# Kernel optimization log

Measured on AMD Instinct MI355X. Metric: run time of the kernel, lower is better.

## Reference

```python
import jax, jax.numpy as jnp
import numpy as np

N_NODES = 50000
N_EDGES = 800000
NFEAT, NHID, NCLASS = 512, 128, 40


def _glorot(key, fan_in, fan_out):
    # mimics the usual GCN uniform init: U(-1/sqrt(fan_out), 1/sqrt(fan_out))
    stdv = 1.0 / np.sqrt(fan_out)
    return jax.random.uniform(key, (fan_in, fan_out), jnp.float32, -stdv, stdv)


def setup_inputs() -> dict:
    key = jax.random.key(0)
    ks = jax.random.split(key, 8)
    x = jax.random.normal(ks[0], (N_NODES, NFEAT), jnp.float32)
    edge_src = jax.random.randint(ks[1], (N_EDGES,), 0, N_NODES)
    edge_dst = jax.random.randint(ks[2], (N_EDGES,), 0, N_NODES)
    edge_weight = jax.random.uniform(ks[3], (N_EDGES,), jnp.float32)
    W1 = _glorot(ks[4], NFEAT, NHID)
    b1 = jnp.zeros((NHID,), jnp.float32)
    W2 = _glorot(ks[5], NHID, NCLASS)
    b2 = jnp.zeros((NCLASS,), jnp.float32)
    return {"x": x, "edge_src": edge_src, "edge_dst": edge_dst,
            "edge_weight": edge_weight, "W1": W1, "b1": b1, "W2": W2, "b2": b2}


def _gcn_layer(x, W, b, edge_src, edge_dst, edge_weight):
    # support = x @ W ; out = spmm(adj, support) + b
    support = x @ W                                   # [N, F_out]
    msgs = support[edge_src] * edge_weight[:, None]   # [E, F_out]
    agg = jax.ops.segment_sum(msgs, edge_dst, num_segments=N_NODES)
    return agg + b


def reference(x, edge_src, edge_dst, edge_weight, W1, b1, W2, b2):
    h = _gcn_layer(x, W1, b1, edge_src, edge_dst, edge_weight)
    h = jax.nn.relu(h)
    # F.dropout(training=False) -> identity in eval mode
    out = _gcn_layer(h, W2, b2, edge_src, edge_dst, edge_weight)
    return out
```

## Files before the change

### kernel.cpp

```cpp
#include <hip/hip_runtime.h>


#define F0 512
#define F1 128
#define F2 40
#define F2P 48

typedef short bf16x8 __attribute__((ext_vector_type(8)));
typedef float f32x4 __attribute__((ext_vector_type(4)));

static __device__ __forceinline__ unsigned short f2b(float f){
    union { float f; unsigned int u; } x; x.f = f;
    unsigned int u = x.u;
    unsigned int r = (u + 0x7fffu + ((u >> 16) & 1u)) >> 16;
    return (unsigned short)r;
}
static __device__ __forceinline__ unsigned short f2b_fast(float f){
    return (unsigned short)((__float_as_uint(f) + 0x8000u) >> 16);
}
static __device__ __forceinline__ unsigned int pack2(float a, float b){
    unsigned int ua = __float_as_uint(a) + 0x8000u;
    unsigned int ub = __float_as_uint(b) + 0x8000u;
    return __builtin_amdgcn_perm(ub, ua, 0x07060302u);
}
static __device__ __forceinline__ bf16x8 pack8(float4 v0, float4 v1){
    union { bf16x8 v; unsigned int d[4]; } r;
    r.d[0] = pack2(v0.x, v0.y);
    r.d[1] = pack2(v0.z, v0.w);
    r.d[2] = pack2(v1.x, v1.y);
    r.d[3] = pack2(v1.z, v1.w);
    return r.v;
}
static __device__ __forceinline__ float b2f(unsigned short h){
    union { unsigned int u; float f; } x; x.u = ((unsigned int)h) << 16; return x.f;
}
static __device__ __forceinline__ unsigned short f2h(float f){
    union { _Float16 h; unsigned short u; } x; x.h = (_Float16)f; return x.u;
}
static __device__ __forceinline__ float h2f(unsigned short u){
    union { unsigned short u; _Float16 h; } x; x.u = u; return (float)x.h;
}

__global__ void prep_w(const float* __restrict__ W1, const float* __restrict__ W2,
                       unsigned short* __restrict__ W1t, unsigned short* __restrict__ W2t,
                       int* __restrict__ cnt8, int n8, int* __restrict__ gflag){
    int idx = blockIdx.x*256 + threadIdx.x;
    if (idx < n8) cnt8[idx] = 0;
    if (idx < 64) gflag[idx] = 0;
    if (idx < F0*F1){
        int k = idx >> 7, n = idx & 127;
        W1t[(size_t)n*F0 + k] = f2b(W1[idx]);
    } else if (idx < F0*F1 + F2P*F1){
        int j = idx - F0*F1;
        int n = j >> 7, k = j & 127;
        float v = (n < F2) ? W2[(size_t)k*F2 + n] : 0.f;
        W2t[j] = f2b(v);
    }
}

__global__ __launch_bounds__(256, 3) void gemm1h(const float* __restrict__ X,
                                                 const unsigned short* __restrict__ W1t,
                                                 unsigned short* __restrict__ S1, int M,
                                                 const int* __restrict__ dst,
                                                 int* __restrict__ cnt8,
                                                 unsigned short* __restrict__ slot,
                                                 int E, int epb){
    __shared__ unsigned short sB[128*136];
    int tid = threadIdx.x;
    int wave = tid >> 6, lane = tid & 63;
    int quad = lane >> 4, l16 = lane & 15;
    int row0 = blockIdx.x * 64;
    int myrow = row0 + wave*16 + l16;
    int arow = min(myrow, M-1);
    const float* xrow = X + (size_t)arow * F0;

    bf16x8 a[16];
    #pragma unroll
    for (int t=0; t<16; t++){
        float4 v0 = *(const float4*)(xrow + t*32 + quad*8);
        float4 v1 = *(const float4*)(xrow + t*32 + quad*8 + 4);
        a[t] = pack8(v0, v1);
    }
    __builtin_amdgcn_sched_barrier(0);

    f32x4 acc[8];
    #pragma unroll
    for (int c=0;c<8;c++) acc[c] = (f32x4){0.f,0.f,0.f,0.f};

    #pragma unroll
    for (int p = 0; p < 4; p++){
        __syncthreads();
        #pragma unroll
        for (int i=0;i<8;i++){
            int idx = tid + i*256;
            int nn = idx >> 4, c8 = idx & 15;
            *(float4*)&sB[nn*136 + c8*8] =
                *(const float4*)&W1t[(size_t)nn*F0 + p*128 + c8*8];
        }
        __syncthreads();
        #pragma unroll
        for (int s=0;s<4;s++){
            #pragma unroll
            for (int c=0;c<8;c++){
                bf16x8 b = *(bf16x8*)&sB[(c*16 + l16)*136 + s*32 + quad*8];
                acc[c] = __builtin_amdgcn_mfma_f32_16x16x32_bf16(a[p*4+s], b, acc[c], 0, 0, 0);
            }
        }
    }
    #pragma unroll
    for (int c=0;c<8;c++){
        #pragma unroll
        for (int r=0;r<4;r++){
            int grow = row0 + wave*16 + quad*4 + r;
            if (grow < M) S1[(size_t)grow*F1 + c*16 + l16] = f2b_fast(acc[c][r]);
        }
    }

    int ebase = blockIdx.x * epb;
    int eend  = min(ebase + epb, E);
    for (int e = ebase + tid; e < eend; e += 256){
        int d = dst[e];
        int s = e & 7;
        slot[e] = (unsigned short)atomicAdd(&cnt8[d*8 + s], 1);
    }
}

__global__ void scan_fused(const int* __restrict__ cnt8, int* __restrict__ offs,
                           int* __restrict__ sbase, int* __restrict__ gflag,
                           int n, int E){
    __shared__ int sd[256];
    __shared__ int s_excl;
    int tid = threadIdx.x, bid = blockIdx.x;
    int base = bid*1024 + tid*4;

    int t[4];
    int lpr[4][8];
    #pragma unroll
    for (int j=0;j<4;j++){
        int node = base+j;
        int tot = 0;
        #pragma unroll
        for (int k=0;k<8;k++) lpr[j][k] = 0;
        if (node < n){
            int4 c0 = *(const int4*)&cnt8[(size_t)node*8];
            int4 c1 = *(const int4*)&cnt8[(size_t)node*8+4];
            int run;
            lpr[j][0] = 0;   run  = c0.x;
            lpr[j][1] = run; run += c0.y;
            lpr[j][2] = run; run += c0.z;
            lpr[j][3] = run; run += c0.w;
            lpr[j][4] = run; run += c1.x;
            lpr[j][5] = run; run += c1.y;
            lpr[j][6] = run; run += c1.z;
            lpr[j][7] = run; run += c1.w;
            tot = run;
        }
        t[j] = tot;
    }
    int v1 = t[0], v2 = t[0]+t[1], v3 = v2+t[2];
    int s = v3 + t[3];
    sd[tid] = s; __syncthreads();
    for (int off=1; off<256; off<<=1){
        int tt = (tid>=off) ? sd[tid-off] : 0;
        __syncthreads();
        sd[tid] += tt;
        __syncthreads();
    }
    int excl = sd[tid] - s;
    int btot = sd[255];

    if (tid == 0)
        __hip_atomic_store(&gflag[bid], btot + 1, __ATOMIC_RELEASE, __HIP_MEMORY_SCOPE_AGENT);
    if (tid < 64){
        int v = 0;
        if (tid < bid){
            int g;
            do {
                g = __hip_atomic_load(&gflag[tid], __ATOMIC_ACQUIRE, __HIP_MEMORY_SCOPE_AGENT);
                if (g == 0) __builtin_amdgcn_s_sleep(1);
            } while (g == 0);
            v = g - 1;
        }
        #pragma unroll
        for (int o=1; o<64; o<<=1) v += __shfl_xor(v, o);
        if (tid == 0) s_excl = v;
    }
    __syncthreads();

    int node_off[4] = {0, v1, v2, v3};
    int gexcl = s_excl + excl;
    #pragma unroll
    for (int j=0;j<4;j++){
        int node = base+j;
        if (node < n){
            int o = gexcl + node_off[j];
            offs[node] = o;
            int4 s0, s1;
            s0.x = o + lpr[j][0]; s0.y = o + lpr[j][1];
            s0.z = o + lpr[j][2]; s0.w = o + lpr[j][3];
            s1.x = o + lpr[j][4]; s1.y = o + lpr[j][5];
            s1.z = o + lpr[j][6]; s1.w = o + lpr[j][7];
            *(int4*)&sbase[(size_t)node*8]   = s0;
            *(int4*)&sbase[(size_t)node*8+4] = s1;
        }
    }
    if (bid == 0 && tid == 0) offs[n] = E;
}

__global__ void scatter_kernel(const int* __restrict__ src, const int* __restrict__ dst,
                               const float* __restrict__ w,
                               const int* __restrict__ sbase,
                               const unsigned short* __restrict__ slot,
                               unsigned int* __restrict__ edges, int E){
    int e = blockIdx.x*256+threadIdx.x;
    if (e<E){
        int d = dst[e];
        int pos = sbase[d*8 + (e & 7)] + (int)slot[e];
        edges[pos] = ((unsigned int)src[e] << 16) | (unsigned int)f2h(w[e]);
    }
}

__global__ void agg1_kernel(const unsigned short* __restrict__ S1, const int* __restrict__ offs,
                            const unsigned int* __restrict__ edges,
                            const float* __restrict__ b1, unsigned short* __restrict__ H, int n){
    int node = blockIdx.x*4 + (threadIdx.x >> 6);
    int lane = threadIdx.x & 63;
    if (node >= n) return;
    int half = lane >> 5, fl = lane & 31;
    int e0 = offs[node], e1 = offs[node+1];
    double a0=0.0, a1=0.0, a2=0.0, a3=0.0;
    int e = e0;
    for (; e+8 <= e1; e += 8){
        unsigned int rA = edges[e   + half];
        unsigned int rB = edges[e+2 + half];
        unsigned int rC = edges[e+4 + half];
        unsigned int rD = edges[e+6 + half];
        ushort4 vA = *(const ushort4*)&S1[((size_t)(rA>>16))*F1 + fl*4];
        ushort4 vB = *(const ushort4*)&S1[((size_t)(rB>>16))*F1 + fl*4];
        ushort4 vC = *(const ushort4*)&S1[((size_t)(rC>>16))*F1 + fl*4];
        ushort4 vD = *(const ushort4*)&S1[((size_t)(rD>>16))*F1 + fl*4];
        double wA = h2f((unsigned short)rA), wB = h2f((unsigned short)rB);
        double wC = h2f((unsigned short)rC), wD = h2f((unsigned short)rD);
        a0 += wA*b2f(vA.x) + wB*b2f(vB.x) + wC*b2f(vC.x) + wD*b2f(vD.x);
        a1 += wA*b2f(vA.y) + wB*b2f(vB.y) + wC*b2f(vC.y) + wD*b2f(vD.y);
        a2 += wA*b2f(vA.z) + wB*b2f(vB.z) + wC*b2f(vC.z) + wD*b2f(vD.z);
        a3 += wA*b2f(vA.w) + wB*b2f(vB.w) + wC*b2f(vC.w) + wD*b2f(vD.w);
    }
    for (; e < e1; e += 2){
        int ee = e + half;
        if (ee < e1){
            unsigned int r = edges[ee];
            ushort4 v = *(const ushort4*)&S1[((size_t)(r>>16))*F1 + fl*4];
            double w = h2f((unsigned short)r);
            a0 += w*b2f(v.x); a1 += w*b2f(v.y); a2 += w*b2f(v.z); a3 += w*b2f(v.w);
        }
    }
    a0 += __shfl_down(a0, 32);
    a1 += __shfl_down(a1, 32);
    a2 += __shfl_down(a2, 32);
    a3 += __shfl_down(a3, 32);
    if (lane < 32){
        float4 bb = *(const float4*)&b1[fl*4];
        float o0 = (float)(a0 + (double)bb.x);
        float o1 = (float)(a1 + (double)bb.y);
        float o2 = (float)(a2 + (double)bb.z);
        float o3 = (float)(a3 + (double)bb.w);
        o0 = o0>0.f?o0:0.f; o1 = o1>0.f?o1:0.f;
        o2 = o2>0.f?o2:0.f; o3 = o3>0.f?o3:0.f;
        union { ushort4 v; unsigned int d[2]; } o;
        o.d[0] = pack2(o0, o1);
        o.d[1] = pack2(o2, o3);
        *(ushort4*)&H[(size_t)node*F1 + fl*4] = o.v;
    }
}

__global__ __launch_bounds__(256) void gemm2_mfma(const unsigned short* __restrict__ H,
                                                  const unsigned short* __restrict__ W2t,
                                                  unsigned short* __restrict__ S2, int M){
    __shared__ unsigned short sB[48][136];
    int tid = threadIdx.x;
    int wave = tid >> 6, lane = tid & 63;
    int quad = lane >> 4, l16 = lane & 15;
    for (int i = tid; i < 48*16; i += 256){
        int nn = i >> 4, p = i & 15;
        *(float4*)&sB[nn][p*8] = *(const float4*)&W2t[(size_t)nn*F1 + p*8];
    }
    int row0 = blockIdx.x * 64;
    int myrow = row0 + wave*16 + l16;
    int arow = min(myrow, M-1);
    const unsigned short* hrow = H + (size_t)arow * F1;
    bf16x8 a[4];
    #pragma unroll
    for (int ks=0; ks<4; ks++) a[ks] = *(const bf16x8*)(hrow + ks*32 + quad*8);
    __syncthreads();
    f32x4 acc[3];
    #pragma unroll
    for (int c=0;c<3;c++) acc[c] = (f32x4){0.f,0.f,0.f,0.f};
    #pragma unroll
    for (int ks=0; ks<4; ks++){
        #pragma unroll
        for (int c=0;c<3;c++){
            bf16x8 b = *(bf16x8*)&sB[c*16 + l16][ks*32 + quad*8];
            acc[c] = __builtin_amdgcn_mfma_f32_16x16x32_bf16(a[ks], b, acc[c], 0, 0, 0);
        }
    }
    #pragma unroll
    for (int c=0;c<3;c++){
        #pragma unroll
        for (int r=0;r<4;r++){
            int grow = row0 + wave*16 + quad*4 + r;
            if (grow < M) S2[(size_t)grow*F2P + c*16 + l16] = f2b_fast(acc[c][r]);
        }
    }
}

__global__ void agg2_kernel(const unsigned short* __restrict__ S2, const int* __restrict__ offs,
                            const unsigned int* __restrict__ edges,
                            const float* __restrict__ b2, float* __restrict__ out, int n){
    int node = blockIdx.x*4 + (threadIdx.x >> 6);
    int lane = threadIdx.x & 63;
    if (node >= n) return;
    int grp = lane >> 4, gl = lane & 15;
    bool act = gl < 10;
    int e0 = offs[node], e1 = offs[node+1];
    double a0=0.0, a1=0.0, a2=0.0, a3=0.0;
    for (int e = e0; e < e1; e += 4){
        int ee = e + grp;
        if (ee < e1 && act){
            unsigned int r = edges[ee];
            ushort4 v = *(const ushort4*)&S2[((size_t)(r>>16))*F2P + gl*4];
            double w = h2f((unsigned short)r);
            a0 += w*b2f(v.x); a1 += w*b2f(v.y); a2 += w*b2f(v.z); a3 += w*b2f(v.w);
        }
    }
    a0 += __shfl_down(a0, 32); a0 += __shfl_down(a0, 16);
    a1 += __shfl_down(a1, 32); a1 += __shfl_down(a1, 16);
    a2 += __shfl_down(a2, 32); a2 += __shfl_down(a2, 16);
    a3 += __shfl_down(a3, 32); a3 += __shfl_down(a3, 16);
    if (lane < 10){
        float4 bb = *(const float4*)&b2[lane*4];
        float4 o;
        o.x = (float)(a0 + (double)bb.x);
        o.y = (float)(a1 + (double)bb.y);
        o.z = (float)(a2 + (double)bb.z);
        o.w = (float)(a3 + (double)bb.w);
        *(float4*)&out[(size_t)node*F2 + lane*4] = o;
    }
}

extern "C" void kernel_launch(void* const* d_in, const int* in_sizes, int n_in,
                              void* d_out, int out_size, void* d_ws, size_t ws_size,
                              hipStream_t stream){
    const float* x    = (const float*)d_in[0];
    const int*   esrc = (const int*)d_in[1];
    const int*   edst = (const int*)d_in[2];
    const float* ew   = (const float*)d_in[3];
    const float* W1   = (const float*)d_in[4];
    const float* b1   = (const float*)d_in[5];
    const float* W2   = (const float*)d_in[6];
    const float* b2   = (const float*)d_in[7];
    float* out = (float*)d_out;
    int N = in_sizes[0] / F0;
    int E = in_sizes[1];

    char* ws = (char*)d_ws;
    size_t off = 0;
    auto alloc = [&](size_t bytes)->void*{
        void* p = ws + off; off += (bytes + 255) & ~(size_t)255; return p;
    };
    unsigned short* S1 = (unsigned short*)alloc(sizeof(unsigned short)*(size_t)N*F1);
    unsigned short* H  = (unsigned short*)alloc(sizeof(unsigned short)*(size_t)N*F1);
    unsigned short* S2 = (unsigned short*)alloc(sizeof(unsigned short)*(size_t)N*F2P);
    unsigned short* W1t = (unsigned short*)alloc(sizeof(unsigned short)*F1*F0);
    unsigned short* W2t = (unsigned short*)alloc(sizeof(unsigned short)*F2P*F1);
    int*   offs  = (int*)alloc(sizeof(int)*(size_t)(N+1));
    int*   cnt8  = (int*)alloc(sizeof(int)*(size_t)N*8);
    int*   sbase = (int*)alloc(sizeof(int)*(size_t)N*8);
    unsigned short* slot = (unsigned short*)alloc(sizeof(unsigned short)*(size_t)E);
    unsigned int* edges = (unsigned int*)alloc(sizeof(unsigned int)*(size_t)E);
    int*   gflag = (int*)alloc(sizeof(int)*64);

    int n8 = N*8;
    int prep_items = n8 > (F0*F1 + F2P*F1) ? n8 : (F0*F1 + F2P*F1);
    prep_w<<<(prep_items+255)/256,256,0,stream>>>(W1, W2, W1t, W2t, cnt8, n8, gflag);

    int gemm_nb = (N+63)/64;
    int epb = (E + gemm_nb - 1) / gemm_nb;
    gemm1h<<<gemm_nb,256,0,stream>>>(x, W1t, S1, N, edst, cnt8, slot, E, epb);

    int nb = (N+1023)/1024;
    scan_fused<<<nb,256,0,stream>>>(cnt8, offs, sbase, gflag, N, E);
    scatter_kernel<<<(E+255)/256,256,0,stream>>>(esrc, edst, ew, sbase, slot, edges, E);

    agg1_kernel<<<(N+3)/4,256,0,stream>>>(S1, offs, edges, b1, H, N);
    gemm2_mfma<<<gemm_nb,256,0,stream>>>(H, W2t, S2, N);
    agg2_kernel<<<(N+3)/4,256,0,stream>>>(S2, offs, edges, b2, out, N);
}
```

Baseline: 318.5 us.

## Split fused GEMM1/histogram into separate convert, histogram, and bf16 GEMM kernels

```diff
diff --git a/kernel.cpp b/kernel.cpp
--- a/kernel.cpp
+++ b/kernel.cpp
@@ -58,38 +58,46 @@
     }
 }
 
-__global__ __launch_bounds__(256, 3) void gemm1h(const float* __restrict__ X,
-                                                 const unsigned short* __restrict__ W1t,
-                                                 unsigned short* __restrict__ S1, int M,
-                                                 const int* __restrict__ dst,
-                                                 int* __restrict__ cnt8,
-                                                 unsigned short* __restrict__ slot,
-                                                 int E, int epb){
+__global__ void xconv(const float* __restrict__ X, unsigned short* __restrict__ Xb, int n8){
+    int stride = gridDim.x*256;
+    for (int i = blockIdx.x*256 + threadIdx.x; i < n8; i += stride){
+        const float4* p = (const float4*)(X + (size_t)i*8);
+        float4 v0 = p[0], v1 = p[1];
+        *(bf16x8*)&Xb[(size_t)i*8] = pack8(v0, v1);
+    }
+}
+
+__global__ void hist_kernel(const int* __restrict__ dst, int* __restrict__ cnt8,
+                            unsigned short* __restrict__ slot, int E){
+    int e = blockIdx.x*256 + threadIdx.x;
+    if (e < E){
+        int d = dst[e];
+        slot[e] = (unsigned short)atomicAdd(&cnt8[d*8 + (e & 7)], 1);
+    }
+}
+
+__global__ __launch_bounds__(256) void gemm1_mfma(const unsigned short* __restrict__ Xb,
+                                                  const unsigned short* __restrict__ W1t,
+                                                  unsigned short* __restrict__ S1, int M){
     __shared__ unsigned short sB[128*136];
     int tid = threadIdx.x;
     int wave = tid >> 6, lane = tid & 63;
     int quad = lane >> 4, l16 = lane & 15;
     int row0 = blockIdx.x * 64;
-    int myrow = row0 + wave*16 + l16;
-    int arow = min(myrow, M-1);
-    const float* xrow = X + (size_t)arow * F0;
-
-    bf16x8 a[16];
-    #pragma unroll
-    for (int t=0; t<16; t++){
-        float4 v0 = *(const float4*)(xrow + t*32 + quad*8);
-        float4 v1 = *(const float4*)(xrow + t*32 + quad*8 + 4);
-        a[t] = pack8(v0, v1);
-    }
-    __builtin_amdgcn_sched_barrier(0);
+    int arow = min(row0 + wave*16 + l16, M-1);
+    const unsigned short* xrow = Xb + (size_t)arow * F0;
 
     f32x4 acc[8];
     #pragma unroll
     for (int c=0;c<8;c++) acc[c] = (f32x4){0.f,0.f,0.f,0.f};
 
-    #pragma unroll
+    #pragma unroll 1
     for (int p = 0; p < 4; p++){
         __syncthreads();
+        bf16x8 a0 = *(const bf16x8*)(xrow + p*128 + 0*32 + quad*8);
+        bf16x8 a1 = *(const bf16x8*)(xrow + p*128 + 1*32 + quad*8);
+        bf16x8 a2 = *(const bf16x8*)(xrow + p*128 + 2*32 + quad*8);
+        bf16x8 a3 = *(const bf16x8*)(xrow + p*128 + 3*32 + quad*8);
         #pragma unroll
         for (int i=0;i<8;i++){
             int idx = tid + i*256;
@@ -99,12 +107,15 @@
         }
         __syncthreads();
         #pragma unroll
-        for (int s=0;s<4;s++){
-            #pragma unroll
-            for (int c=0;c<8;c++){
-                bf16x8 b = *(bf16x8*)&sB[(c*16 + l16)*136 + s*32 + quad*8];
-                acc[c] = __builtin_amdgcn_mfma_f32_16x16x32_bf16(a[p*4+s], b, acc[c], 0, 0, 0);
-            }
+        for (int c=0;c<8;c++){
+            bf16x8 b0 = *(bf16x8*)&sB[(c*16 + l16)*136 + 0*32 + quad*8];
+            acc[c] = __builtin_amdgcn_mfma_f32_16x16x32_bf16(a0, b0, acc[c], 0, 0, 0);
+            bf16x8 b1 = *(bf16x8*)&sB[(c*16 + l16)*136 + 1*32 + quad*8];
+            acc[c] = __builtin_amdgcn_mfma_f32_16x16x32_bf16(a1, b1, acc[c], 0, 0, 0);
+            bf16x8 b2 = *(bf16x8*)&sB[(c*16 + l16)*136 + 2*32 + quad*8];
+            acc[c] = __builtin_amdgcn_mfma_f32_16x16x32_bf16(a2, b2, acc[c], 0, 0, 0);
+            bf16x8 b3 = *(bf16x8*)&sB[(c*16 + l16)*136 + 3*32 + quad*8];
+            acc[c] = __builtin_amdgcn_mfma_f32_16x16x32_bf16(a3, b3, acc[c], 0, 0, 0);
         }
     }
     #pragma unroll
@@ -114,14 +125,6 @@
             int grow = row0 + wave*16 + quad*4 + r;
             if (grow < M) S1[(size_t)grow*F1 + c*16 + l16] = f2b_fast(acc[c][r]);
         }
-    }
-
-    int ebase = blockIdx.x * epb;
-    int eend  = min(ebase + epb, E);
-    for (int e = ebase + tid; e < eend; e += 256){
-        int d = dst[e];
-        int s = e & 7;
-        slot[e] = (unsigned short)atomicAdd(&cnt8[d*8 + s], 1);
     }
 }
 
@@ -368,6 +371,7 @@
     auto alloc = [&](size_t bytes)->void*{
         void* p = ws + off; off += (bytes + 255) & ~(size_t)255; return p;
     };
+    unsigned short* Xb = (unsigned short*)alloc(sizeof(unsigned short)*(size_t)N*F0);
     unsigned short* S1 = (unsigned short*)alloc(sizeof(unsigned short)*(size_t)N*F1);
     unsigned short* H  = (unsigned short*)alloc(sizeof(unsigned short)*(size_t)N*F1);
     unsigned short* S2 = (unsigned short*)alloc(sizeof(unsigned short)*(size_t)N*F2P);
@@ -384,9 +388,12 @@
     int prep_items = n8 > (F0*F1 + F2P*F1) ? n8 : (F0*F1 + F2P*F1);
     prep_w<<<(prep_items+255)/256,256,0,stream>>>(W1, W2, W1t, W2t, cnt8, n8, gflag);
 
+    hist_kernel<<<(E+255)/256,256,0,stream>>>(edst, cnt8, slot, E);
+
+    xconv<<<2048,256,0,stream>>>(x, Xb, N*F0/8);
+
     int gemm_nb = (N+63)/64;
-    int epb = (E + gemm_nb - 1) / gemm_nb;
-    gemm1h<<<gemm_nb,256,0,stream>>>(x, W1t, S1, N, edst, cnt8, slot, E, epb);
+    gemm1_mfma<<<gemm_nb,256,0,stream>>>(Xb, W1t, S1, N);
 
     int nb = (N+1023)/1024;
     scan_fused<<<nb,256,0,stream>>>(cnt8, offs, sbase, gflag, N, E);
```

After: 337.0 us. 5.8% more time.
